# Optimization experiments

Measured on AMD Instinct MI355X. Metric: run time of the kernel, lower is better.

Reference implementation:

```python
import jax, jax.numpy as jnp
import numpy as np

B, S, E = 4, 2048, 1024

def setup_inputs() -> dict:
    key = jax.random.key(0)
    ks = jax.random.split(key, 7)
    s = 1.0 / np.sqrt(E)
    return {
        "x":  jax.random.normal(ks[0], (B, S, E), jnp.float32),
        "Wq": jax.random.normal(ks[1], (E, E), jnp.float32) * s,
        "bq": jax.random.normal(ks[2], (E,), jnp.float32) * s,
        "Wk": jax.random.normal(ks[3], (E, E), jnp.float32) * s,
        "bk": jax.random.normal(ks[4], (E,), jnp.float32) * s,
        "Wv": jax.random.normal(ks[5], (E, E), jnp.float32) * s,
        "bv": jax.random.normal(ks[6], (E,), jnp.float32) * s,
    }

def reference(x, Wq, bq, Wk, bk, Wv, bv):
    # Linear layers: y = x @ W^T + b (torch nn.Linear convention)
    q = jnp.einsum('bse,fe->bsf', x, Wq) + bq
    k = jnp.einsum('bse,fe->bsf', x, Wk) + bk
    v = jnp.einsum('bse,fe->bsf', x, Wv) + bv
    inv_scale = jnp.asarray(E ** 0.5, x.dtype)
    scores = jnp.einsum('bqe,bke->bqk', q, k) / inv_scale  # [B,S,S]
    attn = jax.nn.softmax(scores, axis=-1)
    # dropout is identity in eval mode (deterministic reference)
    out = jnp.einsum('bqk,bke->bqe', attn, v)
    return out
```

## Files before the change

kernel.cpp:

```cpp
#include <hip/hip_runtime.h>
#include <hip/hip_bf16.h>
#include <cstdint>


typedef __attribute__((ext_vector_type(8))) short bf16x8;
typedef __attribute__((ext_vector_type(4))) float f32x4;

__device__ __forceinline__ unsigned short f2bf(float f) {
  union { float f; uint32_t u; } x; x.f = f;
  uint32_t u = x.u;
  return (unsigned short)((u + 0x7fffu + ((u >> 16) & 1u)) >> 16);
}

__device__ __forceinline__ void async_copy16(const void* g, void* l) {
  __builtin_amdgcn_global_load_lds(
      (const __attribute__((address_space(1))) void*)g,
      (__attribute__((address_space(3))) void*)l, 16, 0, 0);
}

__global__ __launch_bounds__(256) void convert_all(
    const float* __restrict__ x, const float* __restrict__ Wq,
    const float* __restrict__ Wk, const float* __restrict__ Wv,
    unsigned short* __restrict__ xb, unsigned short* __restrict__ Wb,
    float* __restrict__ rowsum) {
  const long X4 = (long)8192 * 1024 / 4;
  const long W4 = (long)1024 * 1024 / 4;
  if (blockIdx.x == gridDim.x - 1) {
    float4* r = (float4*)rowsum;
#pragma unroll
    for (int t = 0; t < 8; ++t)
      r[threadIdx.x + t * 256] = float4{0.f, 0.f, 0.f, 0.f};
    return;
  }
  long i = (long)blockIdx.x * 256 + threadIdx.x;
  const float* src; unsigned short* dst; long off;
  if (i < X4)             { src = x;  dst = xb;                    off = i; }
  else if (i < X4 + W4)   { src = Wq; dst = Wb;                    off = i - X4; }
  else if (i < X4 + 2*W4) { src = Wk; dst = Wb + (long)1024*1024;  off = i - X4 - W4; }
  else                    { src = Wv; dst = Wb + (long)2048*1024;  off = i - X4 - 2*W4; }
  const float4 v = ((const float4*)src)[off];
  ushort4 o;
  o.x = f2bf(v.x); o.y = f2bf(v.y); o.z = f2bf(v.z); o.w = f2bf(v.w);
  ((ushort4*)dst)[off] = o;
}

template <int MODE>
__global__ __launch_bounds__(256, 4) void gemm_bt(
    const unsigned short* __restrict__ Ab, const unsigned short* __restrict__ Bb,
    unsigned short* __restrict__ Cb, float* __restrict__ Cf,
    unsigned short* __restrict__ VT,
    const float* __restrict__ bias0, const float* __restrict__ bias1,
    const float* __restrict__ bias2, float* __restrict__ rowsum,
    int K, int N, float scale, long sA, long sB, long sC) {
  __shared__ unsigned short As[128 * 64];
  __shared__ unsigned short Bs[128 * 64];

  const int z = blockIdx.z;
  const unsigned short* A  = Ab + (long)z * sA;
  const unsigned short* Bm = Bb + (long)z * sB;

  const int tid  = threadIdx.x;
  const int lane = tid & 63;
  const int wave = tid >> 6;
  const int l15  = lane & 15;
  const int quad = lane >> 4;
  const int wm = (wave >> 1) * 64;
  const int wn = (wave & 1) * 64;

  const int tile_m = blockIdx.x * 128;
  const int tile_n = blockIdx.y * 128;

  const int rs8 = lane >> 3;
  const int kc  = (lane & 7) ^ rs8;
  const long lK = (long)K;
  const unsigned short* gA0 = A  + (long)(tile_m + wave * 32 + rs8) * lK + kc * 8;
  const unsigned short* gB0 = Bm + (long)(tile_n + wave * 32 + rs8) * lK + kc * 8;
  unsigned short* lA = &As[(wave * 32) * 64];
  unsigned short* lB = &Bs[(wave * 32) * 64];

  const int g0 = (0 * 4 + quad) ^ (l15 & 7);
  const int g1 = (1 * 4 + quad) ^ (l15 & 7);

  f32x4 acc[4][4] = {};

  for (int k0 = 0; k0 < K; k0 += 64) {
    __syncthreads();
#pragma unroll
    for (int t = 0; t < 4; ++t) {
      async_copy16(gA0 + (long)t * 8 * lK + k0, lA + t * 8 * 64);
      async_copy16(gB0 + (long)t * 8 * lK + k0, lB + t * 8 * 64);
    }
    __syncthreads();

#pragma unroll
    for (int s = 0; s < 2; ++s) {
      const int gs = s ? g1 : g0;
      bf16x8 af[4], bfr[4];
#pragma unroll
      for (int i = 0; i < 4; ++i)
        af[i] = *(const bf16x8*)&As[(wm + i * 16 + l15) * 64 + gs * 8];
#pragma unroll
      for (int j = 0; j < 4; ++j)
        bfr[j] = *(const bf16x8*)&Bs[(wn + j * 16 + l15) * 64 + gs * 8];
#pragma unroll
      for (int i = 0; i < 4; ++i)
#pragma unroll
        for (int j = 0; j < 4; ++j)
          acc[i][j] = __builtin_amdgcn_mfma_f32_16x16x32_bf16(af[i], bfr[j], acc[i][j], 0, 0, 0);
    }
  }

  if (MODE == 0) {
    const float* bias = (z == 0) ? bias0 : (z == 1) ? bias1 : bias2;
    if (z == 2) {
#pragma unroll
      for (int j = 0; j < 4; ++j) {
        const int col = tile_n + wn + j * 16 + l15;
        const float bv = bias[col];
#pragma unroll
        for (int i = 0; i < 4; ++i) {
          const int row0 = tile_m + wm + i * 16 + quad * 4;
          const int b = row0 >> 11;
          const int sx = row0 & 2047;
          ushort4 o;
          o.x = f2bf(acc[i][j][0] + bv);
          o.y = f2bf(acc[i][j][1] + bv);
          o.z = f2bf(acc[i][j][2] + bv);
          o.w = f2bf(acc[i][j][3] + bv);
          *(ushort4*)&VT[(long)b * 1024 * 2048 + (long)col * 2048 + sx] = o;
        }
      }
    } else {
      unsigned short* Cbz = Cb + (long)z * sC;
#pragma unroll
      for (int j = 0; j < 4; ++j) {
        const int col = tile_n + wn + j * 16 + l15;
        const float bv = bias[col];
#pragma unroll
        for (int i = 0; i < 4; ++i) {
          const int row0 = tile_m + wm + i * 16 + quad * 4;
#pragma unroll
          for (int r = 0; r < 4; ++r)
            Cbz[(long)(row0 + r) * N + col] = f2bf(acc[i][j][r] + bv);
        }
      }
    }
  } else if (MODE == 1) {
    unsigned short* Cbz = Cb + (long)z * sC;
    float part[16];
#pragma unroll
    for (int t = 0; t < 16; ++t) part[t] = 0.0f;
#pragma unroll
    for (int j = 0; j < 4; ++j) {
      const int col = tile_n + wn + j * 16 + l15;
#pragma unroll
      for (int i = 0; i < 4; ++i) {
        const int row0 = tile_m + wm + i * 16 + quad * 4;
#pragma unroll
        for (int r = 0; r < 4; ++r) {
          const float e = __expf(acc[i][j][r] * scale);
          part[i * 4 + r] += e;
          Cbz[(long)(row0 + r) * N + col] = f2bf(e);
        }
      }
    }
#pragma unroll
    for (int t = 0; t < 16; ++t)
#pragma unroll
      for (int o = 1; o < 16; o <<= 1)
        part[t] += __shfl_xor(part[t], o);
    if (l15 == 0) {
#pragma unroll
      for (int i = 0; i < 4; ++i) {
        const int row0 = tile_m + wm + i * 16 + quad * 4;
#pragma unroll
        for (int r = 0; r < 4; ++r)
          atomicAdd(&rowsum[z * 2048 + row0 + r], part[i * 4 + r]);
      }
    }
  } else {
    float* Cfz = Cf + (long)z * sC;
    float inv[16];
#pragma unroll
    for (int i = 0; i < 4; ++i) {
      const int row0 = tile_m + wm + i * 16 + quad * 4;
#pragma unroll
      for (int r = 0; r < 4; ++r)
        inv[i * 4 + r] = 1.0f / rowsum[z * 2048 + row0 + r];
    }
#pragma unroll
    for (int j = 0; j < 4; ++j) {
      const int col = tile_n + wn + j * 16 + l15;
#pragma unroll
      for (int i = 0; i < 4; ++i) {
        const int row0 = tile_m + wm + i * 16 + quad * 4;
#pragma unroll
        for (int r = 0; r < 4; ++r)
          Cfz[(long)(row0 + r) * N + col] = acc[i][j][r] * inv[i * 4 + r];
      }
    }
  }
}

extern "C" void kernel_launch(void* const* d_in, const int* in_sizes, int n_in,
                              void* d_out, int out_size, void* d_ws, size_t ws_size,
                              hipStream_t stream) {
  const float* x  = (const float*)d_in[0];
  const float* Wq = (const float*)d_in[1];
  const float* bq = (const float*)d_in[2];
  const float* Wk = (const float*)d_in[3];
  const float* bk = (const float*)d_in[4];
  const float* Wv = (const float*)d_in[5];
  const float* bv = (const float*)d_in[6];
  float* out = (float*)d_out;

  constexpr int Bt = 4, S = 2048, E = 1024;
  constexpr int M = Bt * S;

  unsigned short* xb = (unsigned short*)d_ws;
  unsigned short* Wb = xb + (size_t)M * E;
  unsigned short* Q  = Wb + (size_t)3 * E * E;
  unsigned short* Kb = Q + (size_t)M * E;
  unsigned short* VT = Kb + (size_t)M * E;
  unsigned short* P  = VT + (size_t)M * E;
  float* rowsum = (float*)(P + (size_t)Bt * S * S);

  const int conv_blocks = (M * E / 4 + 3 * (E * E / 4)) / 256 + 1;
  convert_all<<<dim3(conv_blocks), dim3(256), 0, stream>>>(x, Wq, Wk, Wv, xb, Wb, rowsum);

  gemm_bt<0><<<dim3(M / 128, E / 128, 3), dim3(256), 0, stream>>>(
      xb, Wb, Q, nullptr, VT, bq, bk, bv, nullptr, E, E, 1.0f,
      0L, (long)E * E, (long)M * E);

  gemm_bt<1><<<dim3(S / 128, S / 128, Bt), dim3(256), 0, stream>>>(
      Q, Kb, P, nullptr, nullptr, nullptr, nullptr, nullptr, rowsum,
      E, S, 1.0f / 32.0f, (long)S * E, (long)S * E, (long)S * S);

  gemm_bt<2><<<dim3(S / 128, E / 128, Bt), dim3(256), 0, stream>>>(
      P, VT, nullptr, out, nullptr, nullptr, nullptr, nullptr, rowsum,
      S, E, 1.0f, (long)S * S, (long)E * S, (long)S * E);
}
```

Measured before the change: 233.3 us.

## Split PV GEMM along K into two halves with atomic accumulation

The final attention-times-V GEMM is split into two K halves, which doubles the grid so more blocks fill the GPU. Partial results are accumulated into the output with float atomicAdd. The output buffer is zeroed by extra blocks in the conversion kernel. In exchange this adds extra output write traffic, atomic overhead and nondeterministic summation order.

```diff
diff --git a/kernel.cpp b/kernel.cpp
--- a/kernel.cpp
+++ b/kernel.cpp
@@ -18,21 +18,30 @@
       (__attribute__((address_space(3))) void*)l, 16, 0, 0);
 }
 
+#define CONV_BLOCKS 11264
 __global__ __launch_bounds__(256) void convert_all(
     const float* __restrict__ x, const float* __restrict__ Wq,
     const float* __restrict__ Wk, const float* __restrict__ Wv,
     unsigned short* __restrict__ xb, unsigned short* __restrict__ Wb,
-    float* __restrict__ rowsum) {
+    float* __restrict__ rowsum, float* __restrict__ outz) {
   const long X4 = (long)8192 * 1024 / 4;
   const long W4 = (long)1024 * 1024 / 4;
-  if (blockIdx.x == gridDim.x - 1) {
-    float4* r = (float4*)rowsum;
-#pragma unroll
-    for (int t = 0; t < 8; ++t)
-      r[threadIdx.x + t * 256] = float4{0.f, 0.f, 0.f, 0.f};
+  const int bid = blockIdx.x;
+  if (bid >= CONV_BLOCKS) {
+    if (bid == gridDim.x - 1) {
+      float4* r = (float4*)rowsum;
+#pragma unroll
+      for (int t = 0; t < 8; ++t)
+        r[threadIdx.x + t * 256] = float4{0.f, 0.f, 0.f, 0.f};
+    } else {
+      float4* o = (float4*)outz + (long)(bid - CONV_BLOCKS) * 1024;
+#pragma unroll
+      for (int t = 0; t < 4; ++t)
+        o[threadIdx.x + t * 256] = float4{0.f, 0.f, 0.f, 0.f};
+    }
     return;
   }
-  long i = (long)blockIdx.x * 256 + threadIdx.x;
+  long i = (long)bid * 256 + threadIdx.x;
   const float* src; unsigned short* dst; long off;
   if (i < X4)             { src = x;  dst = xb;                    off = i; }
   else if (i < X4 + W4)   { src = Wq; dst = Wb;                    off = i - X4; }
@@ -51,13 +60,15 @@
     unsigned short* __restrict__ VT,
     const float* __restrict__ bias0, const float* __restrict__ bias1,
     const float* __restrict__ bias2, float* __restrict__ rowsum,
-    int K, int N, float scale, long sA, long sB, long sC) {
+    int K, int N, float scale, long sA, long sB, long sC, long ldAB) {
   __shared__ unsigned short As[128 * 64];
   __shared__ unsigned short Bs[128 * 64];
 
-  const int z = blockIdx.z;
-  const unsigned short* A  = Ab + (long)z * sA;
-  const unsigned short* Bm = Bb + (long)z * sB;
+  int z = blockIdx.z;
+  long koff = 0;
+  if (MODE == 2) { koff = (long)(z >> 2) * K; z &= 3; }
+  const unsigned short* A  = Ab + (long)z * sA + koff;
+  const unsigned short* Bm = Bb + (long)z * sB + koff;
 
   const int tid  = threadIdx.x;
   const int lane = tid & 63;
@@ -72,7 +83,7 @@
 
   const int rs8 = lane >> 3;
   const int kc  = (lane & 7) ^ rs8;
-  const long lK = (long)K;
+  const long lK = ldAB;
   const unsigned short* gA0 = A  + (long)(tile_m + wave * 32 + rs8) * lK + kc * 8;
   const unsigned short* gB0 = Bm + (long)(tile_n + wave * 32 + rs8) * lK + kc * 8;
   unsigned short* lA = &As[(wave * 32) * 64];
@@ -196,7 +207,8 @@
         const int row0 = tile_m + wm + i * 16 + quad * 4;
 #pragma unroll
         for (int r = 0; r < 4; ++r)
-          Cfz[(long)(row0 + r) * N + col] = acc[i][j][r] * inv[i * 4 + r];
+          atomicAdd(&Cfz[(long)(row0 + r) * N + col],
+                    acc[i][j][r] * inv[i * 4 + r]);
       }
     }
   }
@@ -225,18 +237,18 @@
   unsigned short* P  = VT + (size_t)M * E;
   float* rowsum = (float*)(P + (size_t)Bt * S * S);
 
-  const int conv_blocks = (M * E / 4 + 3 * (E * E / 4)) / 256 + 1;
-  convert_all<<<dim3(conv_blocks), dim3(256), 0, stream>>>(x, Wq, Wk, Wv, xb, Wb, rowsum);
+  convert_all<<<dim3(CONV_BLOCKS + 2048 + 1), dim3(256), 0, stream>>>(
+      x, Wq, Wk, Wv, xb, Wb, rowsum, out);
 
   gemm_bt<0><<<dim3(M / 128, E / 128, 3), dim3(256), 0, stream>>>(
       xb, Wb, Q, nullptr, VT, bq, bk, bv, nullptr, E, E, 1.0f,
-      0L, (long)E * E, (long)M * E);
+      0L, (long)E * E, (long)M * E, (long)E);
 
   gemm_bt<1><<<dim3(S / 128, S / 128, Bt), dim3(256), 0, stream>>>(
       Q, Kb, P, nullptr, nullptr, nullptr, nullptr, nullptr, rowsum,
-      E, S, 1.0f / 32.0f, (long)S * E, (long)S * E, (long)S * S);
-
-  gemm_bt<2><<<dim3(S / 128, E / 128, Bt), dim3(256), 0, stream>>>(
+      E, S, 1.0f / 32.0f, (long)S * E, (long)S * E, (long)S * S, (long)E);
+
+  gemm_bt<2><<<dim3(S / 128, E / 128, 2 * Bt), dim3(256), 0, stream>>>(
       P, VT, nullptr, out, nullptr, nullptr, nullptr, nullptr, rowsum,
-      S, E, 1.0f, (long)S * S, (long)E * S, (long)S * E);
-}
+      S / 2, E, 1.0f, (long)S * S, (long)E * S, (long)S * E, (long)S);
+}
```

After: 273.3 us. +17.2%, slower.
